# Performance work log

Measured on AMD Instinct MI355X. Metric: run time of the kernel, lower is better.

## Reference

```python
import jax, jax.numpy as jnp
import numpy as np

N_NODES = 50000
N_EDGES = 800000
IN_F = 128
OUT_F = 128
HEADS = 8
HEAD_DIM = OUT_F // HEADS
EDGE_F = 64


def setup_inputs() -> dict:
    key = jax.random.key(0)
    ks = jax.random.split(key, 12)
    s = 0.05
    return {
        "node_features": jax.random.normal(ks[0], (N_NODES, IN_F), jnp.float32),
        "edge_index": jax.random.randint(ks[1], (2, N_EDGES), 0, N_NODES, jnp.int32),
        "edge_features": jax.random.normal(ks[2], (N_EDGES, EDGE_F), jnp.float32),
        "Wq": jax.random.normal(ks[3], (IN_F, OUT_F), jnp.float32) * s,
        "bq": jnp.zeros((OUT_F,), jnp.float32),
        "Wk": jax.random.normal(ks[4], (IN_F, OUT_F), jnp.float32) * s,
        "bk": jnp.zeros((OUT_F,), jnp.float32),
        "Wv": jax.random.normal(ks[5], (IN_F, OUT_F), jnp.float32) * s,
        "bv": jnp.zeros((OUT_F,), jnp.float32),
        "We": jax.random.normal(ks[6], (EDGE_F, HEADS), jnp.float32) * s,
        "be": jnp.zeros((HEADS,), jnp.float32),
        "Wo": jax.random.normal(ks[7], (OUT_F, OUT_F), jnp.float32) * s,
        "bo": jnp.zeros((OUT_F,), jnp.float32),
    }


def reference(node_features, edge_index, edge_features,
              Wq, bq, Wk, bk, Wv, bv, We, be, Wo, bo):
    n_nodes = node_features.shape[0]
    scale = HEAD_DIM ** (-0.5)
    sources = edge_index[0]
    targets = edge_index[1]

    q = (node_features @ Wq + bq).reshape(n_nodes, HEADS, HEAD_DIM)
    k = (node_features @ Wk + bk).reshape(n_nodes, HEADS, HEAD_DIM)
    v = (node_features @ Wv + bv).reshape(n_nodes, HEADS, HEAD_DIM)

    # edge-wise gathers: [E, H, D]
    q_t = q[targets]
    k_s = k[sources]
    v_s = v[sources]

    # scores [E, H] with edge bias
    scores = jnp.sum(q_t * k_s, axis=-1) * scale + (edge_features @ We + be)

    # segment softmax over edges sharing a target node
    max_s = jax.ops.segment_max(scores, targets, num_segments=n_nodes)
    e = jnp.exp(scores - max_s[targets])
    denom = jax.ops.segment_sum(e, targets, num_segments=n_nodes) + 1e-10
    probs = e / denom[targets]

    weighted = (probs[:, :, None] * v_s).reshape(scores.shape[0], -1)  # [E, H*D]
    agg = jax.ops.segment_sum(weighted, targets, num_segments=n_nodes)  # [N, H*D]
    return agg @ Wo + bo
```

## Files before the change

### kernel.cpp

```cpp
#include <hip/hip_runtime.h>
#include <hip/hip_bf16.h>
#include <math.h>

#define IN_F   128
#define OUT_F  128
#define HEADS  8
#define HEAD_D 16
#define EDGE_F 64
#define BUCKET 64

typedef __attribute__((ext_vector_type(8))) short bf16x8;
typedef __attribute__((ext_vector_type(4))) float f32x4;

__device__ inline unsigned int f2bf(float f) {
    union { float f; unsigned int u; } c; c.f = f;
    unsigned int r = c.u + 0x7FFFu + ((c.u >> 16) & 1u);
    return r >> 16;
}

__device__ inline int wperm(int col) {
    return (col & 0x70) | ((col & 7) << 1) | ((col >> 3) & 1);
}

__global__ __launch_bounds__(256)
void prep_kernel(const float* __restrict__ Wq, const float* __restrict__ Wk,
                 const float* __restrict__ Wv, const float* __restrict__ Wo,
                 uint4* __restrict__ Wb, int* __restrict__ deg, int n_nodes) {
    int id = blockIdx.x * 256 + threadIdx.x;
    if (id < n_nodes) deg[id] = 0;
    if (id >= 8192) return;
    int lane = id & 63;
    int kb   = (id >> 6) & 3;
    int ct   = (id >> 8) & 7;
    int mat  = id >> 11;
    const float* W = (mat == 0) ? Wq : (mat == 1) ? Wk : (mat == 2) ? Wv : Wo;
    int n  = ct * 16 + (lane & 15);
    int k0 = kb * 32 + (lane >> 4) * 8;
    unsigned int t[8];
    #pragma unroll
    for (int j = 0; j < 8; ++j) t[j] = f2bf(W[(size_t)(k0 + j) * 128 + n]);
    uint4 val;
    val.x = t[0] | (t[1] << 16);
    val.y = t[2] | (t[3] << 16);
    val.z = t[4] | (t[5] << 16);
    val.w = t[6] | (t[7] << 16);
    Wb[id] = val;
}

__global__ __launch_bounds__(256)
void qkv_edges(const float* __restrict__ x, const bf16x8* __restrict__ WbV,
               const float* __restrict__ bq, const float* __restrict__ bk,
               const float* __restrict__ bv,
               float* __restrict__ q, unsigned int* __restrict__ kvp, int n_nodes,
               const float* __restrict__ ef, const float* __restrict__ We,
               const float* __restrict__ be, float* __restrict__ ebias,
               const int* __restrict__ ei, int* __restrict__ deg,
               int2* __restrict__ csr2, int n_edges, int node_blocks) {
    __shared__ float sWe[EDGE_F * 9];
    __shared__ float sbe[HEADS];
    const int tid = threadIdx.x;

    if ((int)blockIdx.x < node_blocks) {
        const int wave = tid >> 6;
        const int lane = tid & 63;
        const int quad = lane >> 4;
        const int lcol = lane & 15;
        const int row0 = blockIdx.x * 64 + wave * 16;
        const int m    = row0 + lcol;

        bf16x8 afrag[4];
        const bool mv = (m < n_nodes);
        const float* xr = x + (size_t)m * IN_F;
        #pragma unroll
        for (int kb = 0; kb < 4; ++kb) {
            float buf[8];
            if (mv) {
                float4 a = ((const float4*)(xr + kb * 32 + quad * 8))[0];
                float4 b = ((const float4*)(xr + kb * 32 + quad * 8 + 4))[0];
                buf[0]=a.x; buf[1]=a.y; buf[2]=a.z; buf[3]=a.w;
                buf[4]=b.x; buf[5]=b.y; buf[6]=b.z; buf[7]=b.w;
            } else {
                #pragma unroll
                for (int j = 0; j < 8; ++j) buf[j] = 0.f;
            }
            bf16x8 f;
            #pragma unroll
            for (int j = 0; j < 8; ++j) f[j] = (short)f2bf(buf[j]);
            afrag[kb] = f;
        }

        #pragma unroll
        for (int ct = 0; ct < 8; ++ct) {
            f32x4 aq = {0.f,0.f,0.f,0.f}, ak = {0.f,0.f,0.f,0.f}, av = {0.f,0.f,0.f,0.f};
            #pragma unroll
            for (int kb = 0; kb < 4; ++kb) {
                bf16x8 bq_ = WbV[((0 * 8 + ct) * 4 + kb) * 64 + lane];
                bf16x8 bk_ = WbV[((1 * 8 + ct) * 4 + kb) * 64 + lane];
                bf16x8 bv_ = WbV[((2 * 8 + ct) * 4 + kb) * 64 + lane];
                aq = __builtin_amdgcn_mfma_f32_16x16x32_bf16(afrag[kb], bq_, aq, 0, 0, 0);
                ak = __builtin_amdgcn_mfma_f32_16x16x32_bf16(afrag[kb], bk_, ak, 0, 0, 0);
                av = __builtin_amdgcn_mfma_f32_16x16x32_bf16(afrag[kb], bv_, av, 0, 0, 0);
            }
            const int col = ct * 16 + lcol;
            const int wcol = wperm(col);
            float bqc = bq[col], bkc = bk[col], bvc = bv[col];
            #pragma unroll
            for (int r = 0; r < 4; ++r) {
                int node = row0 + quad * 4 + r;
                if (node < n_nodes) {
                    q[(size_t)node * OUT_F + col]    = aq[r] + bqc;
                    kvp[(size_t)node * OUT_F + wcol] = f2bf(ak[r] + bkc) | (f2bf(av[r] + bvc) << 16);
                }
            }
        }
    } else {
        #pragma unroll
        for (int i = tid; i < EDGE_F * HEADS; i += 256)
            sWe[(i >> 3) * 9 + (i & 7)] = We[i];
        if (tid < HEADS) sbe[tid] = be[tid];
        __syncthreads();

        const int wave = tid >> 6;
        const int lane = tid & 63;
        const int g    = lane >> 2;
        const int c    = lane & 3;
        const int e    = (blockIdx.x - node_blocks) * 64 + wave * 16 + g;
        const bool ok  = (e < n_edges);

        float4 a0, a1, a2, a3;
        a0 = a1 = a2 = a3 = make_float4(0.f, 0.f, 0.f, 0.f);
        if (ok) {
            const float4* er = (const float4*)(ef + (size_t)e * EDGE_F + c * 16);
            a0 = er[0]; a1 = er[1]; a2 = er[2]; a3 = er[3];
        }

        if (ok && c == 0) {
            int s_ = ei[e];
            int t_ = ei[n_edges + e];
            int pos = atomicAdd(&deg[t_], 1);
            if (pos < BUCKET) csr2[((size_t)t_ << 6) + pos] = make_int2(s_, e);
        }

        float acc[HEADS];
        #pragma unroll
        for (int h = 0; h < HEADS; ++h) acc[h] = 0.f;
        float evv[16] = {a0.x, a0.y, a0.z, a0.w, a1.x, a1.y, a1.z, a1.w,
                         a2.x, a2.y, a2.z, a2.w, a3.x, a3.y, a3.z, a3.w};
        #pragma unroll
        for (int jj = 0; jj < 16; ++jj) {
            #pragma unroll
            for (int h = 0; h < HEADS; ++h)
                acc[h] = fmaf(evv[jj], sWe[(c * 16 + jj) * 9 + h], acc[h]);
        }
        #pragma unroll
        for (int m = 1; m < 4; m <<= 1) {
            #pragma unroll
            for (int h = 0; h < HEADS; ++h)
                acc[h] += __shfl_xor(acc[h], m, 4);
        }
        if (ok) {
            float2 st = make_float2(acc[2 * c]     + sbe[2 * c],
                                    acc[2 * c + 1] + sbe[2 * c + 1]);
            ((float2*)(ebias + (size_t)e * HEADS))[c] = st;
        }
    }
}

__global__ __launch_bounds__(256)
void agg_kernel(const int2* __restrict__ csr2, const int* __restrict__ deg,
                const float* __restrict__ q, const char* __restrict__ kvpb,
                const char* __restrict__ ebiasb, unsigned short* __restrict__ aggn,
                int n_nodes) {
    __shared__ int2 soff[4][BUCKET];
    const int tid  = threadIdx.x;
    const int wave = tid >> 6;
    const int lane = tid & 63;
    const int t    = blockIdx.x * 4 + wave;

    const int h  = lane >> 3;
    const int r  = lane & 7;
    const int fa = h * 16 + r;
    const int kvo_lane = lane << 3;
    const int ebo_lane = h << 2;

    int cnt = 0;
    if (t < n_nodes) {
        cnt = deg[t]; if (cnt > BUCKET) cnt = BUCKET;
        int2 se = csr2[((size_t)t << 6) + lane];
        if (lane >= cnt) se = make_int2(0, 0);
        soff[wave][lane] = make_int2(se.x << 9, se.y << 5);
    }
    __syncthreads();
    if (t >= n_nodes) return;

    const float qa = q[(size_t)t * OUT_F + fa];
    const float qb = q[(size_t)t * OUT_F + fa + 8];

    const int cntR = (cnt + 3) & ~3;

    float acc_a = 0.f, acc_b = 0.f, den = 0.f;

    auto process = [&](unsigned long long kv, float eb) {
        unsigned int w0 = (unsigned int)kv;
        unsigned int w1 = (unsigned int)(kv >> 32);
        float ka = __uint_as_float(w0 << 16);
        float va = __uint_as_float(w0 & 0xFFFF0000u);
        float kb = __uint_as_float(w1 << 16);
        float vb = __uint_as_float(w1 & 0xFFFF0000u);
        float pa = __fmul_rn(qa, ka);
        float pb = __fmul_rn(qb, kb);
        float p  = __fadd_rn(pa, pb);
        p = __fadd_rn(p, __shfl_xor(p, 4, 8));
        p = __fadd_rn(p, __shfl_xor(p, 2, 8));
        p = __fadd_rn(p, __shfl_xor(p, 1, 8));
        float w = __expf(fmaf(p, 0.25f, eb));
        den += w;
        acc_a = fmaf(w, va, acc_a);
        acc_b = fmaf(w, vb, acc_b);
    };

    auto load4 = [&](int base, unsigned long long* kvd, float* ebd) {
        #pragma unroll
        for (int jj = 0; jj < 4; ++jj) {
            int slot = base + jj;
            int2 off = soff[wave][slot];
            unsigned long long kvv =
                *(const unsigned long long*)(kvpb + (size_t)(unsigned)(off.x + kvo_lane));
            float e_ =
                *(const float*)(ebiasb + (size_t)(unsigned)(off.y + ebo_lane));
            kvd[jj] = kvv;
            ebd[jj] = (slot < cnt) ? e_ : -1e30f;
        }
    };

    unsigned long long kvA[4], kvB[4];
    float ebA[4], ebB[4];
    if (cntR > 0) load4(0, kvA, ebA);
    if (cntR > 4) load4(4, kvB, ebB);

    int i = 0;
    while (i + 8 < cntR) {
        unsigned long long nk[4]; float ne[4];
        load4(i + 8, nk, ne);
        #pragma unroll
        for (int jj = 0; jj < 4; ++jj) process(kvA[jj], ebA[jj]);
        #pragma unroll
        for (int jj = 0; jj < 4; ++jj) { kvA[jj] = kvB[jj]; ebA[jj] = ebB[jj]; }
        #pragma unroll
        for (int jj = 0; jj < 4; ++jj) { kvB[jj] = nk[jj]; ebB[jj] = ne[jj]; }
        i += 4;
    }
    if (cntR > 0) {
        #pragma unroll
        for (int jj = 0; jj < 4; ++jj) process(kvA[jj], ebA[jj]);
    }
    if (cntR > 4) {
        #pragma unroll
        for (int jj = 0; jj < 4; ++jj) process(kvB[jj], ebB[jj]);
    }

    float d = den + 1e-10f;
    aggn[(size_t)t * OUT_F + fa]     = (unsigned short)f2bf(acc_a / d);
    aggn[(size_t)t * OUT_F + fa + 8] = (unsigned short)f2bf(acc_b / d);
}

__global__ __launch_bounds__(256)
void out_mfma(const unsigned short* __restrict__ aggn, const bf16x8* __restrict__ WbV,
              const float* __restrict__ bo, float* __restrict__ out, int n_nodes) {
    const int tid  = threadIdx.x;
    const int wave = tid >> 6;
    const int lane = tid & 63;
    const int quad = lane >> 4;
    const int lcol = lane & 15;
    const int row0 = blockIdx.x * 64 + wave * 16;
    const int m    = row0 + lcol;

    bf16x8 afrag[4];
    const bool mv = (m < n_nodes);
    const bf16x8* ar = (const bf16x8*)(aggn + (size_t)m * OUT_F);
    #pragma unroll
    for (int kb = 0; kb < 4; ++kb) {
        if (mv) afrag[kb] = ar[kb * 4 + quad];
        else {
            bf16x8 z;
            #pragma unroll
            for (int j = 0; j < 8; ++j) z[j] = 0;
            afrag[kb] = z;
        }
    }

    #pragma unroll
    for (int ct = 0; ct < 8; ++ct) {
        f32x4 acc = {0.f, 0.f, 0.f, 0.f};
        #pragma unroll
        for (int kb = 0; kb < 4; ++kb) {
            bf16x8 b = WbV[((3 * 8 + ct) * 4 + kb) * 64 + lane];
            acc = __builtin_amdgcn_mfma_f32_16x16x32_bf16(afrag[kb], b, acc, 0, 0, 0);
        }
        const int col = ct * 16 + lcol;
        float boc = bo[col];
        #pragma unroll
        for (int r = 0; r < 4; ++r) {
            int node = row0 + quad * 4 + r;
            if (node < n_nodes) out[(size_t)node * OUT_F + col] = acc[r] + boc;
        }
    }
}

extern "C" void kernel_launch(void* const* d_in, const int* in_sizes, int n_in,
                              void* d_out, int out_size, void* d_ws, size_t ws_size,
                              hipStream_t stream) {
    const float* x  = (const float*)d_in[0];
    const int*   ei = (const int*)  d_in[1];
    const float* ef = (const float*)d_in[2];
    const float* Wq = (const float*)d_in[3];
    const float* bq = (const float*)d_in[4];
    const float* Wk = (const float*)d_in[5];
    const float* bk = (const float*)d_in[6];
    const float* Wv = (const float*)d_in[7];
    const float* bv = (const float*)d_in[8];
    const float* We = (const float*)d_in[9];
    const float* be = (const float*)d_in[10];
    const float* Wo = (const float*)d_in[11];
    const float* bo = (const float*)d_in[12];
    float* out = (float*)d_out;

    const int n_nodes = in_sizes[0] / IN_F;
    const int n_edges = in_sizes[1] / 2;

    char* w = (char*)d_ws;
    float*          q     = (float*)w;          w += (size_t)n_nodes * OUT_F * 4;
    unsigned int*   kvp   = (unsigned int*)w;   w += (size_t)n_nodes * OUT_F * 4;
    unsigned short* aggn  = (unsigned short*)w; w += (size_t)n_nodes * OUT_F * 2;
    uint4*          Wb    = (uint4*)w;          w += (size_t)8192 * 16;
    int*            deg   = (int*)w;            w += (size_t)n_nodes * 4;
    int2*           csr2  = (int2*)w;           w += (size_t)n_nodes * BUCKET * 8;
    float*          ebias = (float*)w;

    {
        int threads_needed = (n_nodes > 8192) ? n_nodes : 8192;
        prep_kernel<<<(threads_needed + 255) / 256, 256, 0, stream>>>(
            Wq, Wk, Wv, Wo, Wb, deg, n_nodes);
    }

    {
        int node_blocks = (n_nodes + 63) / 64;
        int edge_blocks = (n_edges + 63) / 64;
        qkv_edges<<<node_blocks + edge_blocks, 256, 0, stream>>>(
            x, (const bf16x8*)Wb, bq, bk, bv, q, kvp, n_nodes,
            ef, We, be, ebias, ei, deg, csr2, n_edges, node_blocks);
    }

    agg_kernel<<<(n_nodes + 3) / 4, 256, 0, stream>>>(
        csr2, deg, q, (const char*)kvp, (const char*)ebias, aggn, n_nodes);

    out_mfma<<<(n_nodes + 63) / 64, 256, 0, stream>>>(
        aggn, (const bf16x8*)Wb, bo, out, n_nodes);
}
```

Baseline: 459.1 us.

## Make edge-bias blocks persistent grid-stride with register weights and prefetch

The edge-feature projection now runs in a fixed number of persistent blocks that loop over edges with a grid stride. Each lane keeps its 64 weights in registers instead of shared memory, and the next iteration's edge features are prefetched. Edge blocks are scheduled before node blocks, so the memory-bound edge stream starts first and the many short blocks lose their launch and LDS setup cost. In exchange, register pressure rises (64 weight registers plus the prefetch), and the fixed block count may not fill the device the way it was filled before.

```diff
diff --git a/kernel.cpp b/kernel.cpp
--- a/kernel.cpp
+++ b/kernel.cpp
@@ -8,6 +8,7 @@
 #define HEAD_D 16
 #define EDGE_F 64
 #define BUCKET 64
+#define EDGE_BLOCKS 2048
 
 typedef __attribute__((ext_vector_type(8))) short bf16x8;
 typedef __attribute__((ext_vector_type(4))) float f32x4;
@@ -55,17 +56,82 @@
                const float* __restrict__ ef, const float* __restrict__ We,
                const float* __restrict__ be, float* __restrict__ ebias,
                const int* __restrict__ ei, int* __restrict__ deg,
-               int2* __restrict__ csr2, int n_edges, int node_blocks) {
-    __shared__ float sWe[EDGE_F * 9];
-    __shared__ float sbe[HEADS];
+               int2* __restrict__ csr2, int n_edges, int edge_blocks) {
     const int tid = threadIdx.x;
 
-    if ((int)blockIdx.x < node_blocks) {
+    if ((int)blockIdx.x < edge_blocks) {
+        const int wave = tid >> 6;
+        const int lane = tid & 63;
+        const int g    = lane >> 3;
+        const int c    = lane & 7;
+
+        float wr[64];
+        {
+            const float4* Wr = (const float4*)(We + c * 64);
+            #pragma unroll
+            for (int k = 0; k < 16; ++k) {
+                float4 w4 = Wr[k];
+                wr[k * 4 + 0] = w4.x; wr[k * 4 + 1] = w4.y;
+                wr[k * 4 + 2] = w4.z; wr[k * 4 + 3] = w4.w;
+            }
+        }
+        const float bec = be[c];
+
+        const long long stride = (long long)edge_blocks * 32;
+        long long ebase = (long long)blockIdx.x * 32 + wave * 8;
+        long long e     = ebase + g;
+        bool ok = (e < n_edges);
+
+        float4 a0 = make_float4(0.f, 0.f, 0.f, 0.f), a1 = a0;
+        if (ok) {
+            const float4* er = (const float4*)(ef + (size_t)e * EDGE_F + c * 8);
+            a0 = er[0]; a1 = er[1];
+        }
+
+        while (true) {
+            const long long nbase = ebase + stride;
+            const bool okn = (nbase + g < n_edges);
+            float4 n0 = make_float4(0.f, 0.f, 0.f, 0.f), n1 = n0;
+            if (okn) {
+                const float4* er = (const float4*)(ef + (size_t)(e + stride) * EDGE_F + c * 8);
+                n0 = er[0]; n1 = er[1];
+            }
+
+            if (ok && c == 0) {
+                int s_ = ei[e];
+                int t_ = ei[(size_t)n_edges + e];
+                int pos = atomicAdd(&deg[t_], 1);
+                if (pos < BUCKET) csr2[((size_t)t_ << 6) + pos] = make_int2(s_, (int)e);
+            }
+
+            float acc[HEADS];
+            #pragma unroll
+            for (int h = 0; h < HEADS; ++h) acc[h] = 0.f;
+            float ev[8] = {a0.x, a0.y, a0.z, a0.w, a1.x, a1.y, a1.z, a1.w};
+            #pragma unroll
+            for (int jj = 0; jj < 8; ++jj) {
+                #pragma unroll
+                for (int h = 0; h < HEADS; ++h)
+                    acc[h] = fmaf(ev[jj], wr[jj * 8 + h], acc[h]);
+            }
+            #pragma unroll
+            for (int m = 1; m < 8; m <<= 1) {
+                #pragma unroll
+                for (int h = 0; h < HEADS; ++h)
+                    acc[h] += __shfl_xor(acc[h], m, 8);
+            }
+            if (ok) ebias[(size_t)e * HEADS + c] = acc[c] + bec;
+
+            if (nbase >= n_edges) break;
+            ebase = nbase; e += stride; ok = okn;
+            a0 = n0; a1 = n1;
+        }
+    } else {
         const int wave = tid >> 6;
         const int lane = tid & 63;
         const int quad = lane >> 4;
         const int lcol = lane & 15;
-        const int row0 = blockIdx.x * 64 + wave * 16;
+        const int row0 = ((int)blockIdx.x - edge_blocks) * 64 + wave * 16;
         const int m    = row0 + lcol;
 
         bf16x8 afrag[4];
@@ -112,56 +178,6 @@
                     kvp[(size_t)node * OUT_F + wcol] = f2bf(ak[r] + bkc) | (f2bf(av[r] + bvc) << 16);
                 }
             }
-        }
-    } else {
-        #pragma unroll
-        for (int i = tid; i < EDGE_F * HEADS; i += 256)
-            sWe[(i >> 3) * 9 + (i & 7)] = We[i];
-        if (tid < HEADS) sbe[tid] = be[tid];
-        __syncthreads();
-
-        const int wave = tid >> 6;
-        const int lane = tid & 63;
-        const int g    = lane >> 2;
-        const int c    = lane & 3;
-        const int e    = (blockIdx.x - node_blocks) * 64 + wave * 16 + g;
-        const bool ok  = (e < n_edges);
-
-        float4 a0, a1, a2, a3;
-        a0 = a1 = a2 = a3 = make_float4(0.f, 0.f, 0.f, 0.f);
-        if (ok) {
-            const float4* er = (const float4*)(ef + (size_t)e * EDGE_F + c * 16);
-            a0 = er[0]; a1 = er[1]; a2 = er[2]; a3 = er[3];
-        }
-
-        if (ok && c == 0) {
-            int s_ = ei[e];
-            int t_ = ei[n_edges + e];
-            int pos = atomicAdd(&deg[t_], 1);
-            if (pos < BUCKET) csr2[((size_t)t_ << 6) + pos] = make_int2(s_, e);
-        }
-
-        float acc[HEADS];
-        #pragma unroll
-        for (int h = 0; h < HEADS; ++h) acc[h] = 0.f;
-        float evv[16] = {a0.x, a0.y, a0.z, a0.w, a1.x, a1.y, a1.z, a1.w,
-                         a2.x, a2.y, a2.z, a2.w, a3.x, a3.y, a3.z, a3.w};
-        #pragma unroll
-        for (int jj = 0; jj < 16; ++jj) {
-            #pragma unroll
-            for (int h = 0; h < HEADS; ++h)
-                acc[h] = fmaf(evv[jj], sWe[(c * 16 + jj) * 9 + h], acc[h]);
-        }
-        #pragma unroll
-        for (int m = 1; m < 4; m <<= 1) {
-            #pragma unroll
-            for (int h = 0; h < HEADS; ++h)
-                acc[h] += __shfl_xor(acc[h], m, 4);
-        }
-        if (ok) {
-            float2 st = make_float2(acc[2 * c]     + sbe[2 * c],
-                                    acc[2 * c + 1] + sbe[2 * c + 1]);
-            ((float2*)(ebias + (size_t)e * HEADS))[c] = st;
         }
     }
 }
@@ -345,10 +361,9 @@
 
     {
         int node_blocks = (n_nodes + 63) / 64;
-        int edge_blocks = (n_edges + 63) / 64;
-        qkv_edges<<<node_blocks + edge_blocks, 256, 0, stream>>>(
+        qkv_edges<<<EDGE_BLOCKS + node_blocks, 256, 0, stream>>>(
             x, (const bf16x8*)Wb, bq, bk, bv, q, kvp, n_nodes,
-            ef, We, be, ebias, ei, deg, csr2, n_edges, node_blocks);
+            ef, We, be, ebias, ei, deg, csr2, n_edges, EDGE_BLOCKS);
     }
 
     agg_kernel<<<(n_nodes + 3) / 4, 256, 0, stream>>>(
```

Result: no change. 465.3 us (+1.4%).
